# Kernel tuning notes

Measured on AMD Instinct MI355X. Metric: run time of the kernel, lower is better.

The kernel has to match this reference:

```python
import jax, jax.numpy as jnp
import numpy as np

# ---- constants matching init_kwargs ----
ATOM_DIMS = np.array([119, 5, 12, 12, 10, 6, 6, 2, 2])
OFFSETS = np.concatenate([[0], np.cumsum(ATOM_DIMS)[:-1]])  # per-column offsets into concat table
HID = 256
HEADS = 8
BASES = 4
AGGS = 3  # sum, mean, max
LAYERS = 4
FH = HID // HEADS  # 32
N_GRAPHS = 2048
EPS = 1e-5


def setup_inputs() -> dict:
    key = jax.random.key(0)
    ks = iter(jax.random.split(key, 64))
    N, E = 50000, 800000
    x = jax.random.randint(next(ks), (N, 9), 0, 2, dtype=jnp.int64) if jax.config.jax_enable_x64 else jax.random.randint(next(ks), (N, 9), 0, 2, dtype=jnp.int32)
    edge_index = jax.random.randint(next(ks), (2, E), 0, N, dtype=x.dtype)
    batch = jnp.sort(jax.random.randint(next(ks), (N,), 0, N_GRAPHS, dtype=x.dtype))
    s = 0.05
    atom_emb = jax.random.normal(next(ks), (int(ATOM_DIMS.sum()), HID), jnp.float32) * s
    bases_W = jax.random.normal(next(ks), (LAYERS, HID, BASES * FH), jnp.float32) * s
    comb_W = jax.random.normal(next(ks), (LAYERS, HID, HEADS * BASES * AGGS), jnp.float32) * s
    comb_b = jnp.zeros((LAYERS, HEADS * BASES * AGGS), jnp.float32)
    conv_bias = jnp.zeros((LAYERS, HID), jnp.float32)
    bn_gamma = jnp.ones((LAYERS, HID), jnp.float32)
    bn_beta = jnp.zeros((LAYERS, HID), jnp.float32)
    w1 = jax.random.normal(next(ks), (HID, HID // 2), jnp.float32) * s
    g1 = jnp.ones((HID // 2,), jnp.float32)
    b1 = jnp.zeros((HID // 2,), jnp.float32)
    w2 = jax.random.normal(next(ks), (HID // 2, HID // 4), jnp.float32) * s
    g2 = jnp.ones((HID // 4,), jnp.float32)
    b2 = jnp.zeros((HID // 4,), jnp.float32)
    w3 = jax.random.normal(next(ks), (HID // 4, 1), jnp.float32) * s
    b3 = jnp.zeros((1,), jnp.float32)
    return dict(atom_emb=atom_emb, bases_W=bases_W, comb_W=comb_W, comb_b=comb_b,
                conv_bias=conv_bias, bn_gamma=bn_gamma, bn_beta=bn_beta,
                w1=w1, g1=g1, b1=b1, w2=w2, g2=g2, b2=b2, w3=w3, b3=b3,
                x=x, edge_index=edge_index, batch=batch)


def _bn(h, gamma, beta):
    mu = h.mean(0)
    var = h.var(0)
    return (h - mu) * jax.lax.rsqrt(var + EPS) * gamma + beta


def reference(atom_emb, bases_W, comb_W, comb_b, conv_bias, bn_gamma, bn_beta,
              w1, g1, b1, w2, g2, b2, w3, b3, x, edge_index, batch):
    N = x.shape[0]
    offs = jnp.asarray(OFFSETS, dtype=x.dtype)
    # AtomEncoder: sum of per-column embeddings (concat table + offsets)
    h = atom_emb[x + offs[None, :]].sum(axis=1)  # [N, HID]

    # edges with self-loops (EGConv add_self_loops=True); adj_t transposed: row=dst
    loop = jnp.arange(N, dtype=edge_index.dtype)
    dst = jnp.concatenate([edge_index[0], loop])
    src = jnp.concatenate([edge_index[1], loop])
    deg = jax.ops.segment_sum(jnp.ones_like(dst, jnp.float32), dst, num_segments=N)  # >=1

    for l in range(LAYERS):
        bases = h @ bases_W[l]                      # [N, B*FH]
        wts = (h @ comb_W[l] + comb_b[l]).reshape(N, HEADS, AGGS * BASES)
        msgs = bases[src]                            # [E+N, B*FH]
        agg_sum = jax.ops.segment_sum(msgs, dst, num_segments=N)
        agg_mean = agg_sum / deg[:, None]
        agg_max = jax.ops.segment_max(msgs, dst, num_segments=N)
        agg = jnp.stack([agg_sum, agg_mean, agg_max], axis=1)  # [N, A, B*FH]
        agg = agg.reshape(N, AGGS * BASES, FH)
        out = jnp.einsum('nhk,nkd->nhd', wts, agg).reshape(N, HID) + conv_bias[l]
        out = jax.nn.relu(_bn(out, bn_gamma[l], bn_beta[l]))
        h = h + out

    # global mean pool
    gsum = jax.ops.segment_sum(h, batch, num_segments=N_GRAPHS)
    gcnt = jax.ops.segment_sum(jnp.ones((N,), jnp.float32), batch, num_segments=N_GRAPHS)
    g = gsum / jnp.maximum(gcnt, 1.0)[:, None]

    z = jax.nn.relu(_bn(g @ w1, g1, b1))
    z = jax.nn.relu(_bn(z @ w2, g2, b2))
    return z @ w3 + b3
```

## Files before the change

kernel.cpp:

```cpp
#include <hip/hip_runtime.h>
#include <hip/hip_bf16.h>

#define HID 256
#define NGRAPH 2048
#define SNB 768

typedef __attribute__((ext_vector_type(8))) short s16x8;
typedef __attribute__((ext_vector_type(4))) float f32x4v;

__device__ inline short f2b(float f) {
    __hip_bfloat16 b = __float2bfloat16(f);
    return *reinterpret_cast<short*>(&b);
}
__device__ inline float b2f_lo(unsigned int v) {
    return __uint_as_float(v << 16);
}
__device__ inline float b2f_hi(unsigned int v) {
    return __uint_as_float(v & 0xffff0000u);
}

__global__ __launch_bounds__(256) void atom_enc(const int* __restrict__ x,
                                                const float* __restrict__ emb,
                                                float* __restrict__ h,
                                                short* __restrict__ hb, int N) {
    int n = blockIdx.x;
    int c = threadIdx.x;
    if (n >= N) return;
    const int offs[9] = {0, 119, 124, 136, 148, 158, 164, 170, 172};
    float s = 0.f;
#pragma unroll
    for (int j = 0; j < 9; ++j) {
        int row = x[n * 9 + j] + offs[j];
        s += emb[row * 256 + c];
    }
    h[n * 256 + c] = s;
    hb[n * 256 + c] = f2b(s);
}

__global__ void prep_wt(const float* __restrict__ bases_W, const float* __restrict__ comb_W,
                        short* __restrict__ WT) {
    int l = blockIdx.x / 224;
    int n = blockIdx.x % 224;
    int k = threadIdx.x;
    float v = (n < 128) ? bases_W[((size_t)l * 256 + k) * 128 + n]
                        : comb_W[((size_t)l * 256 + k) * 96 + (n - 128)];
    WT[((size_t)l * 224 + n) * 256 + k] = f2b(v);
}

__global__ void init_cnt(int* cnt, int N) {
    int i = blockIdx.x * blockDim.x + threadIdx.x;
    if (i < N) cnt[i] = 1;
}

__global__ void csr_count(const int* __restrict__ ei, int E, int* cnt) {
    int e = blockIdx.x * blockDim.x + threadIdx.x;
    if (e >= E) return;
    atomicAdd(&cnt[ei[e]], 1);
}

__global__ __launch_bounds__(256) void scan_s1(const int* __restrict__ cnt, int* __restrict__ blksum, int N) {
    __shared__ int red[256];
    int base = blockIdx.x * 1024;
    int s = 0;
#pragma unroll
    for (int q = 0; q < 4; ++q) {
        int i = base + threadIdx.x * 4 + q;
        s += (i < N) ? cnt[i] : 0;
    }
    red[threadIdx.x] = s;
    __syncthreads();
    for (int off = 128; off > 0; off >>= 1) {
        if (threadIdx.x < off) red[threadIdx.x] += red[threadIdx.x + off];
        __syncthreads();
    }
    if (threadIdx.x == 0) blksum[blockIdx.x] = red[0];
}

__global__ __launch_bounds__(256) void scan_s2(int* __restrict__ blksum, int nb, int* __restrict__ row_ptr, int N) {
    __shared__ int buf[256];
    int v = (threadIdx.x < nb) ? blksum[threadIdx.x] : 0;
    buf[threadIdx.x] = v;
    __syncthreads();
    for (int off = 1; off < 256; off <<= 1) {
        int t = (threadIdx.x >= off) ? buf[threadIdx.x - off] : 0;
        __syncthreads();
        buf[threadIdx.x] += t;
        __syncthreads();
    }
    if (threadIdx.x < nb) blksum[threadIdx.x] = buf[threadIdx.x] - v;
    if (threadIdx.x == 0) row_ptr[N] = buf[255];
}

__global__ __launch_bounds__(256) void scan_s3(const int* __restrict__ cnt, const int* __restrict__ blksum,
                                               int* __restrict__ row_ptr, int* __restrict__ woff, int N) {
    __shared__ int buf[256];
    int base = blockIdx.x * 1024;
    int i0 = base + threadIdx.x * 4;
    int v[4];
    int s = 0;
#pragma unroll
    for (int q = 0; q < 4; ++q) {
        int i = i0 + q;
        v[q] = (i < N) ? cnt[i] : 0;
        s += v[q];
    }
    buf[threadIdx.x] = s;
    __syncthreads();
    for (int off = 1; off < 256; off <<= 1) {
        int t = (threadIdx.x >= off) ? buf[threadIdx.x - off] : 0;
        __syncthreads();
        buf[threadIdx.x] += t;
        __syncthreads();
    }
    int excl = buf[threadIdx.x] - s + blksum[blockIdx.x];
#pragma unroll
    for (int q = 0; q < 4; ++q) {
        int i = i0 + q;
        if (i < N) { row_ptr[i] = excl; woff[i] = excl; }
        excl += v[q];
    }
}

__global__ void csr_scatter(const int* __restrict__ ei, int E, int N,
                            int* __restrict__ woff, int* __restrict__ srcs) {
    int i0 = (blockIdx.x * blockDim.x + threadIdx.x) * 4;
    int T = E + N;
    int d[4], s[4], pos[4];
    bool ok[4];
#pragma unroll
    for (int q = 0; q < 4; ++q) {
        int i = i0 + q;
        ok[q] = (i < T);
        if (ok[q]) {
            if (i < E) { d[q] = ei[i]; s[q] = ei[E + i]; }
            else       { d[q] = i - E; s[q] = i - E; }
        }
    }
#pragma unroll
    for (int q = 0; q < 4; ++q)
        if (ok[q]) pos[q] = atomicAdd(&woff[d[q]], 1);
#pragma unroll
    for (int q = 0; q < 4; ++q)
        if (ok[q]) srcs[pos[q]] = s[q];
}

__global__ __launch_bounds__(256) void gemm_mfma(const short* __restrict__ hb,
                                                 const short* __restrict__ WT,
                                                 const float* __restrict__ cb,
                                                 short* __restrict__ bases,
                                                 float* __restrict__ wts, int N) {
    __shared__ short bs[2][32 * 256];
    int tid = threadIdx.x;
    int wid = tid >> 6;
    int lane = tid & 63;
    int m0 = blockIdx.x * 64 + wid * 16;
    int row_a = m0 + (lane & 15);
    if (row_a > N - 1) row_a = N - 1;
    int kgrp = (lane >> 4) * 8;

    s16x8 a[8];
#pragma unroll
    for (int i = 0; i < 8; ++i)
        a[i] = *(const s16x8*)&hb[(size_t)row_a * 256 + i * 32 + kgrp];

    int st_col = tid >> 3;
    int st_kk = (tid & 7) * 32;
    int st_sw = (st_col & 7) << 4;
    int st_base = st_col * 512 + st_kk * 2;

    auto stage = [&](int buf, int t) {
        const s16x8* src = (const s16x8*)&WT[(size_t)(t * 32 + st_col) * 256 + st_kk];
        char* dst = (char*)bs[buf];
#pragma unroll
        for (int q = 0; q < 4; ++q)
            *(s16x8*)(dst + ((st_base + q * 16) ^ st_sw)) = src[q];
    };

    stage(0, 0);

    int col = lane & 15;
    int rd_base = col * 512 + (lane >> 4) * 16;
    int rd_sw = (col & 7) << 4;
    int rbase = m0 + (lane >> 4) * 4;

    for (int t = 0; t < 7; ++t) {
        __syncthreads();
        if (t + 1 < 7) stage((t + 1) & 1, t + 1);

        const char* base = (const char*)bs[t & 1];
        f32x4v c0 = {0.f, 0.f, 0.f, 0.f};
        f32x4v c1 = {0.f, 0.f, 0.f, 0.f};
#pragma unroll
        for (int i = 0; i < 8; ++i) {
            s16x8 b0 = *(const s16x8*)(base + ((rd_base + i * 64) ^ rd_sw));
            s16x8 b1 = *(const s16x8*)(base + ((rd_base + 8192 + i * 64) ^ rd_sw));
            c0 = __builtin_amdgcn_mfma_f32_16x16x32_bf16(a[i], b0, c0, 0, 0, 0);
            c1 = __builtin_amdgcn_mfma_f32_16x16x32_bf16(a[i], b1, c1, 0, 0, 0);
        }

        int cc0 = t * 32 + col;
        int cc1 = cc0 + 16;
        float cb0 = (cc0 >= 128) ? cb[cc0 - 128] : 0.f;
        float cb1 = (cc1 >= 128) ? cb[cc1 - 128] : 0.f;
#pragma unroll
        for (int r = 0; r < 4; ++r) {
            int row = rbase + r;
            if (row >= N) continue;
            float v0 = c0[r], v1 = c1[r];
            if (cc0 < 128) bases[(size_t)row * 128 + cc0] = f2b(v0);
            else wts[(size_t)row * 96 + (cc0 - 128)] = v0 + cb0;
            if (cc1 < 128) bases[(size_t)row * 128 + cc1] = f2b(v1);
            else wts[(size_t)row * 96 + (cc1 - 128)] = v1 + cb1;
        }
    }
}

__global__ __launch_bounds__(256) void agg_einsum(const short* __restrict__ bases,
                                                  const float* __restrict__ wts,
                                                  const int* __restrict__ row_ptr,
                                                  const int* __restrict__ srcs,
                                                  const float* __restrict__ cbias,
                                                  float* __restrict__ outp, int N) {
    __shared__ float agg_lds[4][3][128];
    __shared__ float wts_lds[4][96];
    int wid = threadIdx.x >> 6;
    int lane = threadIdx.x & 63;
    int n = blockIdx.x * 4 + wid;
    if (n >= N) return;

    int r0 = row_ptr[n];
    int r1 = row_ptr[n + 1];

    wts_lds[wid][lane] = wts[(size_t)n * 96 + lane];
    if (lane < 32) wts_lds[wid][64 + lane] = wts[(size_t)n * 96 + 64 + lane];

    int g = lane & 31;
    int half = lane >> 5;
    const short* bp = bases + 4 * g;
    const float NI = -3.402823466e+38f;
    float sA0 = 0.f, sA1 = 0.f, sA2 = 0.f, sA3 = 0.f;
    float sB0 = 0.f, sB1 = 0.f, sB2 = 0.f, sB3 = 0.f;
    float mA0 = NI, mA1 = NI, mA2 = NI, mA3 = NI;
    float mB0 = NI, mB1 = NI, mB2 = NI, mB3 = NI;

#define GACC8(S, s0_, s1_, s2_, s3_, m0_, m1_, m2_, m3_)                     \
    {                                                                        \
        uint2 v = *(const uint2*)&bp[(size_t)(S) * 128];                     \
        float f0 = b2f_lo(v.x), f1 = b2f_hi(v.x);                            \
        float f2 = b2f_lo(v.y), f3 = b2f_hi(v.y);                            \
        s0_ += f0; s1_ += f1; s2_ += f2; s3_ += f3;                          \
        m0_ = fmaxf(m0_, f0); m1_ = fmaxf(m1_, f1);                          \
        m2_ = fmaxf(m2_, f2); m3_ = fmaxf(m3_, f3);                          \
    }

    int r = r0;
    while (r < r1) {
        int chunk = r1 - r;
        if (chunk > 64) chunk = 64;
        int sidx = (lane < chunk) ? srcs[r + lane] : 0;
        int npair = chunk >> 1;
        int jp = 0;
        for (; jp + 4 <= npair; jp += 4) {
            int e0 = (jp + 0) * 2 + half, e1 = (jp + 1) * 2 + half;
            int e2 = (jp + 2) * 2 + half, e3 = (jp + 3) * 2 + half;
            int s0 = __shfl(sidx, e0), s1 = __shfl(sidx, e1);
            int s2 = __shfl(sidx, e2), s3 = __shfl(sidx, e3);
            GACC8(s0, sA0, sA1, sA2, sA3, mA0, mA1, mA2, mA3);
            GACC8(s1, sB0, sB1, sB2, sB3, mB0, mB1, mB2, mB3);
            GACC8(s2, sA0, sA1, sA2, sA3, mA0, mA1, mA2, mA3);
            GACC8(s3, sB0, sB1, sB2, sB3, mB0, mB1, mB2, mB3);
        }
        for (; jp < npair; ++jp) {
            int e0 = jp * 2 + half;
            int s0 = __shfl(sidx, e0);
            GACC8(s0, sA0, sA1, sA2, sA3, mA0, mA1, mA2, mA3);
        }
        if (chunk & 1) {
            int s0 = __shfl(sidx, chunk - 1);
            if (half == 0) {
                GACC8(s0, sB0, sB1, sB2, sB3, mB0, mB1, mB2, mB3);
            }
        }
        r += chunk;
    }
#undef GACC8

    float s0 = sA0 + sB0, s1 = sA1 + sB1, s2 = sA2 + sB2, s3 = sA3 + sB3;
    float m0 = fmaxf(mA0, mB0), m1 = fmaxf(mA1, mB1);
    float m2 = fmaxf(mA2, mB2), m3 = fmaxf(mA3, mB3);
    s0 += __shfl_xor(s0, 32); s1 += __shfl_xor(s1, 32);
    s2 += __shfl_xor(s2, 32); s3 += __shfl_xor(s3, 32);
    m0 = fmaxf(m0, __shfl_xor(m0, 32)); m1 = fmaxf(m1, __shfl_xor(m1, 32));
    m2 = fmaxf(m2, __shfl_xor(m2, 32)); m3 = fmaxf(m3, __shfl_xor(m3, 32));

    float inv = 1.0f / (float)(r1 - r0);
    if (half == 0) {
        float4 sv = make_float4(s0, s1, s2, s3);
        float4 mv = make_float4(s0 * inv, s1 * inv, s2 * inv, s3 * inv);
        float4 xv = make_float4(m0, m1, m2, m3);
        *(float4*)&agg_lds[wid][0][4 * g] = sv;
        *(float4*)&agg_lds[wid][1][4 * g] = mv;
        *(float4*)&agg_lds[wid][2][4 * g] = xv;
    }

    asm volatile("s_waitcnt lgkmcnt(0)" ::: "memory");

#pragma unroll
    for (int j = 0; j < 4; ++j) {
        int o = lane + 64 * j;
        int hh = o >> 5;
        int d = o & 31;
        float acc = cbias[o];
#pragma unroll
        for (int k = 0; k < 12; ++k)
            acc = fmaf(wts_lds[wid][hh * 12 + k], agg_lds[wid][k >> 2][(k & 3) * 32 + d], acc);
        outp[n * 256 + o] = acc;
    }
}

__global__ __launch_bounds__(256) void bn_stats256(const float4* __restrict__ v, int N,
                                                   float* __restrict__ partial) {
    __shared__ float red[4][2][256];
    int wid = threadIdx.x >> 6;
    int lane = threadIdx.x & 63;
    float4 s = {0.f, 0.f, 0.f, 0.f}, s2 = {0.f, 0.f, 0.f, 0.f};
    int nb = gridDim.x;
    for (int r = blockIdx.x * 8 + wid * 2; r < N; r += nb * 8) {
        float4 t0 = v[(size_t)r * 64 + lane];
        int r1 = r + 1;
        if (r1 < N) {
            float4 t1 = v[(size_t)r1 * 64 + lane];
            s.x += t1.x; s.y += t1.y; s.z += t1.z; s.w += t1.w;
            s2.x += t1.x * t1.x; s2.y += t1.y * t1.y; s2.z += t1.z * t1.z; s2.w += t1.w * t1.w;
        }
        s.x += t0.x; s.y += t0.y; s.z += t0.z; s.w += t0.w;
        s2.x += t0.x * t0.x; s2.y += t0.y * t0.y; s2.z += t0.z * t0.z; s2.w += t0.w * t0.w;
    }
    *(float4*)&red[wid][0][lane * 4] = s;
    *(float4*)&red[wid][1][lane * 4] = s2;
    __syncthreads();
    int c = threadIdx.x;
    float ps = (red[0][0][c] + red[1][0][c]) + (red[2][0][c] + red[3][0][c]);
    float ps2 = (red[0][1][c] + red[1][1][c]) + (red[2][1][c] + red[3][1][c]);
    partial[(blockIdx.x * 2 + 0) * 256 + c] = ps;
    partial[(blockIdx.x * 2 + 1) * 256 + c] = ps2;
}

__global__ void bn_stats(const float* __restrict__ v, int N, int C, float* __restrict__ partial) {
    int c = threadIdx.x;
    float s = 0.f, s2 = 0.f;
    for (int r = blockIdx.x; r < N; r += gridDim.x) {
        float t = v[r * C + c];
        s += t; s2 += t * t;
    }
    partial[(blockIdx.x * 2 + 0) * C + c] = s;
    partial[(blockIdx.x * 2 + 1) * C + c] = s2;
}

__global__ __launch_bounds__(256) void bn_finalize(const float* __restrict__ partial, int NB, int C, int N,
                                                   const float* __restrict__ gamma, const float* __restrict__ beta,
                                                   float* __restrict__ ss) {
    int c = blockIdx.x;
    float s = 0.f, s2 = 0.f;
    for (int b = threadIdx.x; b < NB; b += 256) {
        s += partial[(b * 2 + 0) * C + c];
        s2 += partial[(b * 2 + 1) * C + c];
    }
#pragma unroll
    for (int off = 32; off > 0; off >>= 1) {
        s += __shfl_down(s, off);
        s2 += __shfl_down(s2, off);
    }
    __shared__ float wsum[4][2];
    int wid = threadIdx.x >> 6;
    int lane = threadIdx.x & 63;
    if (lane == 0) { wsum[wid][0] = s; wsum[wid][1] = s2; }
    __syncthreads();
    if (threadIdx.x == 0) {
        s = (wsum[0][0] + wsum[1][0]) + (wsum[2][0] + wsum[3][0]);
        s2 = (wsum[0][1] + wsum[1][1]) + (wsum[2][1] + wsum[3][1]);
        float invN = 1.0f / (float)N;
        float mu = s * invN;
        float var = fmaxf(s2 * invN - mu * mu, 0.f);
        float sc = gamma[c] * rsqrtf(var + 1e-5f);
        ss[c] = sc;
        ss[C + c] = beta[c] - mu * sc;
    }
}

__global__ void bn_apply_res4(float4* __restrict__ h, const float4* __restrict__ outp,
                              const float* __restrict__ ss, short* __restrict__ hb, int total4) {
    int i = blockIdx.x * blockDim.x + threadIdx.x;
    if (i >= total4) return;
    int c0 = (i * 4) & 255;
    float4 o = outp[i];
    float4 hv = h[i];
    hv.x += fmaxf(o.x * ss[c0 + 0] + ss[256 + c0 + 0], 0.f);
    hv.y += fmaxf(o.y * ss[c0 + 1] + ss[256 + c0 + 1], 0.f);
    hv.z += fmaxf(o.z * ss[c0 + 2] + ss[256 + c0 + 2], 0.f);
    hv.w += fmaxf(o.w * ss[c0 + 3] + ss[256 + c0 + 3], 0.f);
    h[i] = hv;
    short4 hb4;
    hb4.x = f2b(hv.x); hb4.y = f2b(hv.y); hb4.z = f2b(hv.z); hb4.w = f2b(hv.w);
    *(short4*)&hb[(size_t)i * 4] = hb4;
}

__global__ void bn_apply(float* __restrict__ z, const float* __restrict__ ss, int total, int C, int Cmask) {
    int i = blockIdx.x * blockDim.x + threadIdx.x;
    if (i >= total) return;
    int c = i & Cmask;
    z[i] = fmaxf(z[i] * ss[c] + ss[C + c], 0.f);
}

__device__ int lower_bound_dev(const int* a, int n, int v) {
    int lo = 0, hi = n;
    while (lo < hi) {
        int mid = (lo + hi) >> 1;
        if (a[mid] < v) lo = mid + 1; else hi = mid;
    }
    return lo;
}

__global__ __launch_bounds__(256) void pool_kernel(const float* __restrict__ h,
                                                   const int* __restrict__ batch, int N,
                                                   float* __restrict__ g) {
    __shared__ int sh[2];
    if (threadIdx.x == 0) {
        sh[0] = lower_bound_dev(batch, N, (int)blockIdx.x);
        sh[1] = lower_bound_dev(batch, N, (int)blockIdx.x + 1);
    }
    __syncthreads();
    int s0 = sh[0], s1 = sh[1];
    float s = 0.f;
    for (int r = s0; r < s1; ++r) s += h[r * 256 + threadIdx.x];
    float cnt = (float)(s1 - s0);
    g[blockIdx.x * 256 + threadIdx.x] = s / fmaxf(cnt, 1.0f);
}

__global__ void mlp_gemm(const float* __restrict__ in, const float* __restrict__ W,
                         float* __restrict__ outp, int K, int C) {
    extern __shared__ float srow[];
    int r = blockIdx.x;
    for (int k = threadIdx.x; k < K; k += blockDim.x) srow[k] = in[r * K + k];
    __syncthreads();
    int c = threadIdx.x;
    float acc = 0.f;
    for (int k = 0; k < K; ++k) acc = fmaf(srow[k], W[k * C + c], acc);
    outp[r * C + c] = acc;
}

__global__ void final_gemm(const float* __restrict__ z2, const float* __restrict__ w3,
                           const float* __restrict__ b3, float* __restrict__ outp, int G) {
    int g = blockIdx.x * blockDim.x + threadIdx.x;
    if (g >= G) return;
    float acc = b3[0];
    for (int k = 0; k < 64; ++k) acc = fmaf(z2[g * 64 + k], w3[k], acc);
    outp[g] = acc;
}

extern "C" void kernel_launch(void* const* d_in, const int* in_sizes, int n_in,
                              void* d_out, int out_size, void* d_ws, size_t ws_size,
                              hipStream_t stream) {
    const float* atom_emb = (const float*)d_in[0];
    const float* bases_W = (const float*)d_in[1];
    const float* comb_W = (const float*)d_in[2];
    const float* comb_b = (const float*)d_in[3];
    const float* conv_bias = (const float*)d_in[4];
    const float* bn_gamma = (const float*)d_in[5];
    const float* bn_beta = (const float*)d_in[6];
    const float* w1 = (const float*)d_in[7];
    const float* g1 = (const float*)d_in[8];
    const float* b1 = (const float*)d_in[9];
    const float* w2 = (const float*)d_in[10];
    const float* g2 = (const float*)d_in[11];
    const float* b2 = (const float*)d_in[12];
    const float* w3 = (const float*)d_in[13];
    const float* b3 = (const float*)d_in[14];
    const int* x = (const int*)d_in[15];
    const int* edge_index = (const int*)d_in[16];
    const int* batch = (const int*)d_in[17];
    float* out = (float*)d_out;

    const int N = in_sizes[15] / 9;
    const int E = in_sizes[16] / 2;
    const int G = NGRAPH;
    const int NCHUNK = (N + 1023) / 1024;

    char* p = (char*)d_ws;
    auto alloc = [&](size_t bytes) -> void* {
        void* r = (void*)p;
        p += (bytes + 255) & ~(size_t)255;
        return r;
    };
    float* h = (float*)alloc((size_t)N * 256 * 4);
    short* hb = (short*)alloc((size_t)N * 256 * 2);
    float* outb = (float*)alloc((size_t)N * 256 * 4);
    short* bases = (short*)alloc((size_t)N * 128 * 2);
    float* wts = (float*)alloc((size_t)N * 96 * 4);
    short* WT = (short*)alloc((size_t)4 * 224 * 256 * 2);
    int* row_ptr = (int*)alloc((size_t)(N + 1) * 4);
    int* cnt = (int*)alloc((size_t)N * 4);
    int* woff = (int*)alloc((size_t)N * 4);
    int* blksum = (int*)alloc((size_t)256 * 4);
    int* srcs = (int*)alloc((size_t)(E + N) * 4);
    float* partial = (float*)alloc((size_t)SNB * 2 * 256 * 4);
    float* ss = (float*)alloc((size_t)2 * 256 * 4);
    float* g = (float*)alloc((size_t)G * 256 * 4);
    float* z1 = (float*)alloc((size_t)G * 128 * 4);
    float* z2 = (float*)alloc((size_t)G * 64 * 4);

    atom_enc<<<N, 256, 0, stream>>>(x, atom_emb, h, hb, N);
    prep_wt<<<4 * 224, 256, 0, stream>>>(bases_W, comb_W, WT);

    init_cnt<<<(N + 255) / 256, 256, 0, stream>>>(cnt, N);
    csr_count<<<(E + 255) / 256, 256, 0, stream>>>(edge_index, E, cnt);
    scan_s1<<<NCHUNK, 256, 0, stream>>>(cnt, blksum, N);
    scan_s2<<<1, 256, 0, stream>>>(blksum, NCHUNK, row_ptr, N);
    scan_s3<<<NCHUNK, 256, 0, stream>>>(cnt, blksum, row_ptr, woff, N);
    csr_scatter<<<(E + N + 1023) / 1024, 256, 0, stream>>>(edge_index, E, N, woff, srcs);

    for (int l = 0; l < 4; ++l) {
        const short* WTl = WT + (size_t)l * 224 * 256;
        const float* cb = comb_b + (size_t)l * 96;
        const float* cbias = conv_bias + (size_t)l * 256;
        const float* gam = bn_gamma + (size_t)l * 256;
        const float* bet = bn_beta + (size_t)l * 256;

        gemm_mfma<<<(N + 63) / 64, 256, 0, stream>>>(hb, WTl, cb, bases, wts, N);
        agg_einsum<<<(N + 3) / 4, 256, 0, stream>>>(bases, wts, row_ptr, srcs, cbias, outb, N);
        bn_stats256<<<SNB, 256, 0, stream>>>((const float4*)outb, N, partial);
        bn_finalize<<<256, 256, 0, stream>>>(partial, SNB, 256, N, gam, bet, ss);
        int total4 = N * 256 / 4;
        bn_apply_res4<<<(total4 + 255) / 256, 256, 0, stream>>>((float4*)h, (const float4*)outb, ss, hb, total4);
    }

    pool_kernel<<<G, 256, 0, stream>>>(h, batch, N, g);

    mlp_gemm<<<G, 128, 256 * 4, stream>>>(g, w1, z1, 256, 128);
    bn_stats<<<64, 128, 0, stream>>>(z1, G, 128, partial);
    bn_finalize<<<128, 256, 0, stream>>>(partial, 64, 128, G, g1, b1, ss);
    bn_apply<<<(G * 128 + 255) / 256, 256, 0, stream>>>(z1, ss, G * 128, 128, 127);

    mlp_gemm<<<G, 64, 128 * 4, stream>>>(z1, w2, z2, 128, 64);
    bn_stats<<<64, 64, 0, stream>>>(z2, G, 64, partial);
    bn_finalize<<<64, 256, 0, stream>>>(partial, 64, 64, G, g2, b2, ss);
    bn_apply<<<(G * 64 + 255) / 256, 256, 0, stream>>>(z2, ss, G * 64, 64, 63);

    final_gemm<<<(G + 255) / 256, 256, 0, stream>>>(z2, w3, b3, out, G);
}
```

Measured before the change: 599.8 us.

## Sort CSR sources via two-level bucket sort, fuse BN stats into aggregation

Replaces the atomic-scatter CSR build with a two-pass bucketed placement that groups edges by destination block, then places them within each bucket using shared-memory atomics. This makes source order deterministic and sorted by destination, which should improve gather locality. BN statistics are now computed inside the aggregation kernel as per-block partials, removing a separate full read of the output buffer, though bn_finalize now reduces over many more partials. The bf16 copy of h is skipped after the last layer.

```diff
diff --git a/kernel.cpp b/kernel.cpp
--- a/kernel.cpp
+++ b/kernel.cpp
@@ -3,7 +3,6 @@
 
 #define HID 256
 #define NGRAPH 2048
-#define SNB 768
 
 typedef __attribute__((ext_vector_type(8))) short s16x8;
 typedef __attribute__((ext_vector_type(4))) float f32x4v;
@@ -121,27 +120,61 @@
     }
 }
 
-__global__ void csr_scatter(const int* __restrict__ ei, int E, int N,
-                            int* __restrict__ woff, int* __restrict__ srcs) {
-    int i0 = (blockIdx.x * blockDim.x + threadIdx.x) * 4;
-    int T = E + N;
-    int d[4], s[4], pos[4];
-    bool ok[4];
-#pragma unroll
-    for (int q = 0; q < 4; ++q) {
-        int i = i0 + q;
-        ok[q] = (i < T);
-        if (ok[q]) {
-            if (i < E) { d[q] = ei[i]; s[q] = ei[E + i]; }
-            else       { d[q] = i - E; s[q] = i - E; }
-        }
-    }
-#pragma unroll
-    for (int q = 0; q < 4; ++q)
-        if (ok[q]) pos[q] = atomicAdd(&woff[d[q]], 1);
-#pragma unroll
-    for (int q = 0; q < 4; ++q)
-        if (ok[q]) srcs[pos[q]] = s[q];
+__global__ __launch_bounds__(256) void ph_hist(const int* __restrict__ ei, int E, int T,
+                                               int PB, int NBK, int* __restrict__ mcnt) {
+    __shared__ int hist[256];
+    hist[threadIdx.x] = 0;
+    __syncthreads();
+    int base = blockIdx.x * 4096;
+#pragma unroll
+    for (int q = 0; q < 16; ++q) {
+        int i = base + q * 256 + threadIdx.x;
+        if (i < T) {
+            int d = (i < E) ? ei[i] : (i - E);
+            atomicAdd(&hist[d >> 8], 1);
+        }
+    }
+    __syncthreads();
+    if (threadIdx.x < NBK) mcnt[threadIdx.x * PB + blockIdx.x] = hist[threadIdx.x];
+}
+
+__global__ __launch_bounds__(256) void ph_scatter(const int* __restrict__ ei, int E, int T,
+                                                  int PB, int NBK, const int* __restrict__ moff,
+                                                  uint2* __restrict__ pairs) {
+    __shared__ int off[256];
+    if (threadIdx.x < NBK) off[threadIdx.x] = moff[threadIdx.x * PB + blockIdx.x];
+    __syncthreads();
+    int base = blockIdx.x * 4096;
+#pragma unroll
+    for (int q = 0; q < 16; ++q) {
+        int i = base + q * 256 + threadIdx.x;
+        if (i < T) {
+            int d, s;
+            if (i < E) { d = ei[i]; s = ei[E + i]; }
+            else       { d = i - E; s = i - E; }
+            int pos = atomicAdd(&off[d >> 8], 1);
+            pairs[pos] = make_uint2((unsigned)d, (unsigned)s);
+        }
+    }
+}
+
+__global__ __launch_bounds__(256) void ph_sort(const uint2* __restrict__ pairs,
+                                               const int* __restrict__ row_ptr,
+                                               const int* __restrict__ moff,
+                                               int NBK, int PB, int T,
+                                               int* __restrict__ srcs) {
+    __shared__ int wcnt[256];
+    wcnt[threadIdx.x] = 0;
+    __syncthreads();
+    int bin = blockIdx.x;
+    int p0 = moff[bin * PB];
+    int p1 = (bin + 1 < NBK) ? moff[(bin + 1) * PB] : T;
+    for (int i = p0 + threadIdx.x; i < p1; i += 256) {
+        uint2 u = pairs[i];
+        int d = (int)u.x;
+        int rank = atomicAdd(&wcnt[d & 255], 1);
+        srcs[row_ptr[d] + rank] = (int)u.y;
+    }
 }
 
 __global__ __launch_bounds__(256) void gemm_mfma(const short* __restrict__ hb,
@@ -220,19 +253,23 @@
                                                   const int* __restrict__ row_ptr,
                                                   const int* __restrict__ srcs,
                                                   const float* __restrict__ cbias,
-                                                  float* __restrict__ outp, int N) {
+                                                  float* __restrict__ outp,
+                                                  float* __restrict__ partial, int N) {
     __shared__ float agg_lds[4][3][128];
     __shared__ float wts_lds[4][96];
+    __shared__ float red[4][256];
     int wid = threadIdx.x >> 6;
     int lane = threadIdx.x & 63;
     int n = blockIdx.x * 4 + wid;
-    if (n >= N) return;
-
-    int r0 = row_ptr[n];
-    int r1 = row_ptr[n + 1];
-
-    wts_lds[wid][lane] = wts[(size_t)n * 96 + lane];
-    if (lane < 32) wts_lds[wid][64 + lane] = wts[(size_t)n * 96 + 64 + lane];
+    bool valid = (n < N);
+
+    int r0 = 0, r1 = 0;
+    if (valid) {
+        r0 = row_ptr[n];
+        r1 = row_ptr[n + 1];
+        wts_lds[wid][lane] = wts[(size_t)n * 96 + lane];
+        if (lane < 32) wts_lds[wid][64 + lane] = wts[(size_t)n * 96 + 64 + lane];
+    }
 
     int g = lane & 31;
     int half = lane >> 5;
@@ -285,65 +322,50 @@
     }
 #undef GACC8
 
-    float s0 = sA0 + sB0, s1 = sA1 + sB1, s2 = sA2 + sB2, s3 = sA3 + sB3;
-    float m0 = fmaxf(mA0, mB0), m1 = fmaxf(mA1, mB1);
-    float m2 = fmaxf(mA2, mB2), m3 = fmaxf(mA3, mB3);
-    s0 += __shfl_xor(s0, 32); s1 += __shfl_xor(s1, 32);
-    s2 += __shfl_xor(s2, 32); s3 += __shfl_xor(s3, 32);
-    m0 = fmaxf(m0, __shfl_xor(m0, 32)); m1 = fmaxf(m1, __shfl_xor(m1, 32));
-    m2 = fmaxf(m2, __shfl_xor(m2, 32)); m3 = fmaxf(m3, __shfl_xor(m3, 32));
-
-    float inv = 1.0f / (float)(r1 - r0);
-    if (half == 0) {
-        float4 sv = make_float4(s0, s1, s2, s3);
-        float4 mv = make_float4(s0 * inv, s1 * inv, s2 * inv, s3 * inv);
-        float4 xv = make_float4(m0, m1, m2, m3);
-        *(float4*)&agg_lds[wid][0][4 * g] = sv;
-        *(float4*)&agg_lds[wid][1][4 * g] = mv;
-        *(float4*)&agg_lds[wid][2][4 * g] = xv;
-    }
-
-    asm volatile("s_waitcnt lgkmcnt(0)" ::: "memory");
-
-#pragma unroll
-    for (int j = 0; j < 4; ++j) {
-        int o = lane + 64 * j;
-        int hh = o >> 5;
-        int d = o & 31;
-        float acc = cbias[o];
-#pragma unroll
-        for (int k = 0; k < 12; ++k)
-            acc = fmaf(wts_lds[wid][hh * 12 + k], agg_lds[wid][k >> 2][(k & 3) * 32 + d], acc);
-        outp[n * 256 + o] = acc;
-    }
-}
-
-__global__ __launch_bounds__(256) void bn_stats256(const float4* __restrict__ v, int N,
-                                                   float* __restrict__ partial) {
-    __shared__ float red[4][2][256];
-    int wid = threadIdx.x >> 6;
-    int lane = threadIdx.x & 63;
-    float4 s = {0.f, 0.f, 0.f, 0.f}, s2 = {0.f, 0.f, 0.f, 0.f};
-    int nb = gridDim.x;
-    for (int r = blockIdx.x * 8 + wid * 2; r < N; r += nb * 8) {
-        float4 t0 = v[(size_t)r * 64 + lane];
-        int r1 = r + 1;
-        if (r1 < N) {
-            float4 t1 = v[(size_t)r1 * 64 + lane];
-            s.x += t1.x; s.y += t1.y; s.z += t1.z; s.w += t1.w;
-            s2.x += t1.x * t1.x; s2.y += t1.y * t1.y; s2.z += t1.z * t1.z; s2.w += t1.w * t1.w;
-        }
-        s.x += t0.x; s.y += t0.y; s.z += t0.z; s.w += t0.w;
-        s2.x += t0.x * t0.x; s2.y += t0.y * t0.y; s2.z += t0.z * t0.z; s2.w += t0.w * t0.w;
-    }
-    *(float4*)&red[wid][0][lane * 4] = s;
-    *(float4*)&red[wid][1][lane * 4] = s2;
+    float accs[4] = {0.f, 0.f, 0.f, 0.f};
+    if (valid) {
+        float s0 = sA0 + sB0, s1 = sA1 + sB1, s2 = sA2 + sB2, s3 = sA3 + sB3;
+        float m0 = fmaxf(mA0, mB0), m1 = fmaxf(mA1, mB1);
+        float m2 = fmaxf(mA2, mB2), m3 = fmaxf(mA3, mB3);
+        s0 += __shfl_xor(s0, 32); s1 += __shfl_xor(s1, 32);
+        s2 += __shfl_xor(s2, 32); s3 += __shfl_xor(s3, 32);
+        m0 = fmaxf(m0, __shfl_xor(m0, 32)); m1 = fmaxf(m1, __shfl_xor(m1, 32));
+        m2 = fmaxf(m2, __shfl_xor(m2, 32)); m3 = fmaxf(m3, __shfl_xor(m3, 32));
+
+        float inv = 1.0f / (float)(r1 - r0);
+        if (half == 0) {
+            float4 sv = make_float4(s0, s1, s2, s3);
+            float4 mv = make_float4(s0 * inv, s1 * inv, s2 * inv, s3 * inv);
+            float4 xv = make_float4(m0, m1, m2, m3);
+            *(float4*)&agg_lds[wid][0][4 * g] = sv;
+            *(float4*)&agg_lds[wid][1][4 * g] = mv;
+            *(float4*)&agg_lds[wid][2][4 * g] = xv;
+        }
+
+        asm volatile("s_waitcnt lgkmcnt(0)" ::: "memory");
+
+#pragma unroll
+        for (int j = 0; j < 4; ++j) {
+            int o = lane + 64 * j;
+            int hh = o >> 5;
+            int d = o & 31;
+            float acc = cbias[o];
+#pragma unroll
+            for (int k = 0; k < 12; ++k)
+                acc = fmaf(wts_lds[wid][hh * 12 + k], agg_lds[wid][k >> 2][(k & 3) * 32 + d], acc);
+            outp[n * 256 + o] = acc;
+            accs[j] = acc;
+        }
+    }
+#pragma unroll
+    for (int j = 0; j < 4; ++j) red[wid][lane + 64 * j] = accs[j];
     __syncthreads();
     int c = threadIdx.x;
-    float ps = (red[0][0][c] + red[1][0][c]) + (red[2][0][c] + red[3][0][c]);
-    float ps2 = (red[0][1][c] + red[1][1][c]) + (red[2][1][c] + red[3][1][c]);
-    partial[(blockIdx.x * 2 + 0) * 256 + c] = ps;
-    partial[(blockIdx.x * 2 + 1) * 256 + c] = ps2;
+    float s = (red[0][c] + red[1][c]) + (red[2][c] + red[3][c]);
+    float s2 = (red[0][c] * red[0][c] + red[1][c] * red[1][c]) +
+               (red[2][c] * red[2][c] + red[3][c] * red[3][c]);
+    partial[((size_t)blockIdx.x * 2 + 0) * 256 + c] = s;
+    partial[((size_t)blockIdx.x * 2 + 1) * 256 + c] = s2;
 }
 
 __global__ void bn_stats(const float* __restrict__ v, int N, int C, float* __restrict__ partial) {
@@ -363,8 +385,8 @@
     int c = blockIdx.x;
     float s = 0.f, s2 = 0.f;
     for (int b = threadIdx.x; b < NB; b += 256) {
-        s += partial[(b * 2 + 0) * C + c];
-        s2 += partial[(b * 2 + 1) * C + c];
+        s += partial[((size_t)b * 2 + 0) * C + c];
+        s2 += partial[((size_t)b * 2 + 1) * C + c];
     }
 #pragma unroll
     for (int off = 32; off > 0; off >>= 1) {
@@ -389,7 +411,8 @@
 }
 
 __global__ void bn_apply_res4(float4* __restrict__ h, const float4* __restrict__ outp,
-                              const float* __restrict__ ss, short* __restrict__ hb, int total4) {
+                              const float* __restrict__ ss, short* __restrict__ hb,
+                              int total4, int write_hb) {
     int i = blockIdx.x * blockDim.x + threadIdx.x;
     if (i >= total4) return;
     int c0 = (i * 4) & 255;
@@ -400,9 +423,11 @@
     hv.z += fmaxf(o.z * ss[c0 + 2] + ss[256 + c0 + 2], 0.f);
     hv.w += fmaxf(o.w * ss[c0 + 3] + ss[256 + c0 + 3], 0.f);
     h[i] = hv;
-    short4 hb4;
-    hb4.x = f2b(hv.x); hb4.y = f2b(hv.y); hb4.z = f2b(hv.z); hb4.w = f2b(hv.w);
-    *(short4*)&hb[(size_t)i * 4] = hb4;
+    if (write_hb) {
+        short4 hb4;
+        hb4.x = f2b(hv.x); hb4.y = f2b(hv.y); hb4.z = f2b(hv.z); hb4.w = f2b(hv.w);
+        *(short4*)&hb[(size_t)i * 4] = hb4;
+    }
 }
 
 __global__ void bn_apply(float* __restrict__ z, const float* __restrict__ ss, int total, int C, int Cmask) {
@@ -484,7 +509,13 @@
     const int N = in_sizes[15] / 9;
     const int E = in_sizes[16] / 2;
     const int G = NGRAPH;
+    const int T = E + N;
     const int NCHUNK = (N + 1023) / 1024;
+    const int PB = (T + 4095) / 4096;
+    const int NBK = (N + 255) >> 8;
+    const int M = NBK * PB;
+    const int MCHUNK = (M + 1023) / 1024;
+    const int AGG_NB = (N + 3) / 4;
 
     char* p = (char*)d_ws;
     auto alloc = [&](size_t bytes) -> void* {
@@ -502,12 +533,15 @@
     int* cnt = (int*)alloc((size_t)N * 4);
     int* woff = (int*)alloc((size_t)N * 4);
     int* blksum = (int*)alloc((size_t)256 * 4);
-    int* srcs = (int*)alloc((size_t)(E + N) * 4);
-    float* partial = (float*)alloc((size_t)SNB * 2 * 256 * 4);
+    int* mcnt = (int*)alloc((size_t)(M + 1) * 4);
+    int* moff = (int*)alloc((size_t)(M + 1) * 4);
+    int* srcs = (int*)alloc((size_t)T * 4);
+    float* partial = (float*)alloc((size_t)AGG_NB * 2 * 256 * 4);
     float* ss = (float*)alloc((size_t)2 * 256 * 4);
     float* g = (float*)alloc((size_t)G * 256 * 4);
     float* z1 = (float*)alloc((size_t)G * 128 * 4);
     float* z2 = (float*)alloc((size_t)G * 64 * 4);
+    uint2* pairs = (uint2*)outb;
 
     atom_enc<<<N, 256, 0, stream>>>(x, atom_emb, h, hb, N);
     prep_wt<<<4 * 224, 256, 0, stream>>>(bases_W, comb_W, WT);
@@ -517,7 +551,13 @@
     scan_s1<<<NCHUNK, 256, 0, stream>>>(cnt, blksum, N);
     scan_s2<<<1, 256, 0, stream>>>(blksum, NCHUNK, row_ptr, N);
     scan_s3<<<NCHUNK, 256, 0, stream>>>(cnt, blksum, row_ptr, woff, N);
-    csr_scatter<<<(E + N + 1023) / 1024, 256, 0, stream>>>(edge_index, E, N, woff, srcs);
+
+    ph_hist<<<PB, 256, 0, stream>>>(edge_index, E, T, PB, NBK, mcnt);
+    scan_s1<<<MCHUNK, 256, 0, stream>>>(mcnt, blksum, M);
+    scan_s2<<<1, 256, 0, stream>>>(blksum, MCHUNK, moff, M);
+    scan_s3<<<MCHUNK, 256, 0, stream>>>(mcnt, blksum, moff, moff, M);
+    ph_scatter<<<PB, 256, 0, stream>>>(edge_index, E, T, PB, NBK, moff, pairs);
+    ph_sort<<<NBK, 256, 0, stream>>>(pairs, row_ptr, moff, NBK, PB, T, srcs);
 
     for (int l = 0; l < 4; ++l) {
         const short* WTl = WT + (size_t)l * 224 * 256;
@@ -527,11 +567,11 @@
         const float* bet = bn_beta + (size_t)l * 256;
 
         gemm_mfma<<<(N + 63) / 64, 256, 0, stream>>>(hb, WTl, cb, bases, wts, N);
-        agg_einsum<<<(N + 3) / 4, 256, 0, stream>>>(bases, wts, row_ptr, srcs, cbias, outb, N);
-        bn_stats256<<<SNB, 256, 0, stream>>>((const float4*)outb, N, partial);
-        bn_finalize<<<256, 256, 0, stream>>>(partial, SNB, 256, N, gam, bet, ss);
+        agg_einsum<<<AGG_NB, 256, 0, stream>>>(bases, wts, row_ptr, srcs, cbias, outb, partial, N);
+        bn_finalize<<<256, 256, 0, stream>>>(partial, AGG_NB, 256, N, gam, bet, ss);
         int total4 = N * 256 / 4;
-        bn_apply_res4<<<(total4 + 255) / 256, 256, 0, stream>>>((float4*)h, (const float4*)outb, ss, hb, total4);
+        bn_apply_res4<<<(total4 + 255) / 256, 256, 0, stream>>>((float4*)h, (const float4*)outb, ss, hb,
+                                                                total4, l < 3 ? 1 : 0);
     }
 
     pool_kernel<<<G, 256, 0, stream>>>(h, batch, N, g);
```

New measurement: 748.4 us. 1.25x slower.
